# Optimization experiments

Hardware: AMD Instinct MI355X
Metric: run time of the kernel (lower is better)

Reference implementation:

```python
import jax, jax.numpy as jnp
import numpy as np

B, S, HID = 1, 2048, 1024
H, HKV, D = 16, 4, 64
THETA = 10000.0


def _rope_tables(seq_len, head_dim):
    # Matches RotaryEmbedding: emb = cat(freqs, freqs); kernel reads cos/sin at even
    # positions d for each rotated pair (d, d+1), i.e. columns 0::2 of the table.
    inv_freq = 1.0 / (THETA ** (jnp.arange(0, head_dim, 2, dtype=jnp.float32) / head_dim))
    freqs = jnp.arange(seq_len, dtype=jnp.float32)[:, None] * inv_freq[None, :]  # [S, D/2]
    emb = jnp.concatenate([freqs, freqs], axis=-1)  # [S, D]
    return jnp.cos(emb)[:, 0::2], jnp.sin(emb)[:, 0::2]  # each [S, D/2]


def _apply_rope(x, cos, sin):
    # x: [B, H, S, D]; rotate interleaved pairs (2i, 2i+1) as in the kernel.
    xe, xo = x[..., 0::2], x[..., 1::2]
    re = xe * cos - xo * sin
    ro = xe * sin + xo * cos
    return jnp.stack([re, ro], axis=-1).reshape(x.shape)


def setup_inputs() -> dict:
    key = jax.random.key(0)
    k0, k1, k2, k3, k4 = jax.random.split(key, 5)
    return {
        "hidden_states": jax.random.normal(k0, (B, S, HID), dtype=jnp.float32),
        "Wq": jax.random.normal(k1, (HID, H * D), dtype=jnp.float32) * 0.02,
        "Wk": jax.random.normal(k2, (HID, HKV * D), dtype=jnp.float32) * 0.02,
        "Wv": jax.random.normal(k3, (HID, HKV * D), dtype=jnp.float32) * 0.02,
        "Wo": jax.random.normal(k4, (H * D, HID), dtype=jnp.float32) * 0.02,
    }


def reference(hidden_states, Wq, Wk, Wv, Wo):
    b, s, _ = hidden_states.shape
    q = (hidden_states @ Wq).reshape(b, s, H, D).transpose(0, 2, 1, 3)    # [B,H,S,D]
    k = (hidden_states @ Wk).reshape(b, s, HKV, D).transpose(0, 2, 1, 3)  # [B,Hkv,S,D]
    v = (hidden_states @ Wv).reshape(b, s, HKV, D).transpose(0, 2, 1, 3)

    cos, sin = _rope_tables(s, D)
    q = _apply_rope(q, cos, sin)
    k = _apply_rope(k, cos, sin)

    G = H // HKV  # GQA group size: query head h -> kv head h // G
    qg = q.reshape(b, HKV, G, s, D)
    scale = jnp.float32(D) ** -0.5
    scores = jnp.einsum("bkgqd,bkpd->bkgqp", qg, k) * scale  # [B,Hkv,G,S,S]
    causal = jnp.tril(jnp.ones((s, s), dtype=bool))
    scores = jnp.where(causal, scores, jnp.float32(-1e30))
    probs = jax.nn.softmax(scores, axis=-1)
    out = jnp.einsum("bkgqp,bkpd->bkgqd", probs, v).reshape(b, H, s, D)
    out = out.transpose(0, 2, 1, 3).reshape(b, s, H * D)
    return out @ Wo
```

## Files before the change

kernel.cpp:

```cpp
#include <hip/hip_runtime.h>
#include <hip/hip_bf16.h>
#include <math.h>

#define SEQ   2048
#define HID   1024
#define NH    16
#define NKV   4
#define DH    64
#define GQ    (NH / NKV)
#define NQKV  1536
#define LQKV  1536
#define KT    64
#define QB    32
#define CH    512
#define NCH   (SEQ / CH)
#define PSTR  72

typedef __attribute__((ext_vector_type(8))) short bf16x8;
typedef __attribute__((ext_vector_type(4))) float f32x4;
typedef unsigned short u16;
typedef unsigned int u32;

__device__ __forceinline__ u16 f2bf(float f) {
    union { float f; unsigned u; } x; x.f = f;
    unsigned r = x.u + 0x7fffu + ((x.u >> 16) & 1u);
    return (u16)(r >> 16);
}
__device__ __forceinline__ u32 pk2bf(float lo, float hi) {
    return (u32)f2bf(lo) | ((u32)f2bf(hi) << 16);
}
__device__ __forceinline__ void load_lds16(const u16* g, u16* l) {
    __builtin_amdgcn_global_load_lds(
        (const __attribute__((address_space(1))) unsigned int*)g,
        (__attribute__((address_space(3))) unsigned int*)l, 16, 0, 0);
}

__global__ __launch_bounds__(256) void setup(const float* __restrict__ X,
                                             const float* __restrict__ Wq,
                                             const float* __restrict__ Wk,
                                             const float* __restrict__ Wv,
                                             const float* __restrict__ Wo,
                                             u16* __restrict__ Xb,
                                             u16* __restrict__ Wt,
                                             u16* __restrict__ WoT) {
    const int z = blockIdx.z;
    if (z == 4) {
        const int idx = ((int)blockIdx.y * 64 + (int)blockIdx.x) * 256 + threadIdx.x;
        const float4 v = ((const float4*)X)[idx];
        ushort4 o;
        o.x = f2bf(v.x); o.y = f2bf(v.y); o.z = f2bf(v.z); o.w = f2bf(v.w);
        ((ushort4*)Xb)[idx] = o;
        return;
    }
    const float* in; u16* out; int N;
    if (z == 0)      { in = Wq; out = Wt;                             N = HID; }
    else if (z == 1) { in = Wk; out = Wt + (size_t)HID * HID;         N = 256; }
    else if (z == 2) { in = Wv; out = Wt + (size_t)(HID + 256) * HID; N = 256; }
    else             { in = Wo; out = WoT;                            N = HID; }

    const int n0 = blockIdx.x * 32;
    if (n0 >= N) return;
    const int k0 = blockIdx.y * 32;

    __shared__ float t[32][33];
    const int tx = threadIdx.x & 31;
    const int ty = threadIdx.x >> 5;
    #pragma unroll
    for (int i = 0; i < 4; ++i)
        t[ty + i * 8][tx] = in[(size_t)(k0 + ty + i * 8) * N + n0 + tx];
    __syncthreads();
    #pragma unroll
    for (int i = 0; i < 4; ++i)
        out[(size_t)(n0 + ty + i * 8) * HID + k0 + tx] = f2bf(t[tx][ty + i * 8]);
}

__global__ __launch_bounds__(256) void gemm64(const u16* __restrict__ A,
                                              const u16* __restrict__ Bt,
                                              float* __restrict__ C,
                                              int K, int ldc) {
    __shared__ u16 Bs[2][64 * 32];

    const int tid  = threadIdx.x;
    const int lane = tid & 63;
    const int w    = tid >> 6;
    const int c    = lane & 15;
    const int quad = lane >> 4;
    const int m0   = blockIdx.y * 64;
    const int n0   = blockIdx.x * 64;

    const u16* gB  = Bt + (size_t)(n0 + w * 16 + (lane >> 2)) * K + (lane & 3) * 8;
    u16* const bdst = (u16*)&Bs[0][0] + (w * 16) * 32;

    const u16* gA = A + (size_t)(m0 + w * 16 + c) * K + quad * 8;

    const int T = K / 32;

    f32x4 acc[4];
    #pragma unroll
    for (int nt = 0; nt < 4; ++nt) acc[nt] = (f32x4){0.f, 0.f, 0.f, 0.f};

    bf16x8 afc, afn;
    afc = *(const bf16x8*)gA;
    load_lds16(gB, bdst);

    for (int t = 0; t < T; ++t) {
        __syncthreads();
        if (t + 1 < T) {
            load_lds16(gB + (t + 1) * 32, bdst + ((t + 1) & 1) * (64 * 32));
            afn = *(const bf16x8*)(gA + (t + 1) * 32);
        }
        bf16x8 bfr[4];
        #pragma unroll
        for (int nt = 0; nt < 4; ++nt)
            bfr[nt] = *(const bf16x8*)&Bs[t & 1][(nt * 16 + c) * 32 + quad * 8];
        #pragma unroll
        for (int nt = 0; nt < 4; ++nt)
            acc[nt] = __builtin_amdgcn_mfma_f32_16x16x32_bf16(afc, bfr[nt], acc[nt], 0, 0, 0);
        afc = afn;
    }

    #pragma unroll
    for (int nt = 0; nt < 4; ++nt)
        #pragma unroll
        for (int rg = 0; rg < 4; ++rg)
            C[(size_t)(m0 + w * 16 + quad * 4 + rg) * ldc + n0 + nt * 16 + c] = acc[nt][rg];
}

__global__ __launch_bounds__(256) void postprocess(const float* __restrict__ QKV,
                                                   u16* __restrict__ Qb,
                                                   u16* __restrict__ Kb,
                                                   u16* __restrict__ VTg) {
    const int s   = blockIdx.x;
    const int tid = threadIdx.x;
    const float* row = QKV + (size_t)s * LQKV;
    const float ln_scale = 9.210340371976184f / 32.0f;

    #pragma unroll
    for (int it = 0; it < 2; ++it) {
        const int p = tid + it * 256;
        const int j = p & 31;
        const float inv_freq = __expf(-(float)((2 * j) & 31) * ln_scale);
        float sn, cs;
        __sincosf((float)s * inv_freq, &sn, &cs);
        const float xe = row[2 * p], xo = row[2 * p + 1];
        Qb[(size_t)s * HID + 2 * p]     = f2bf((xe * cs - xo * sn) * 0.125f);
        Qb[(size_t)s * HID + 2 * p + 1] = f2bf((xe * sn + xo * cs) * 0.125f);
    }
    if (tid < 128) {
        const int p  = tid;
        const int j  = p & 31;
        const int kh = p >> 5;
        const int d  = (2 * p) & 63;
        const float inv_freq = __expf(-(float)((2 * j) & 31) * ln_scale);
        float sn, cs;
        __sincosf((float)s * inv_freq, &sn, &cs);
        const float xe = row[1024 + 2 * p], xo = row[1024 + 2 * p + 1];
        u16* kr = Kb + ((size_t)kh * SEQ + s) * DH;
        kr[d]     = f2bf(xe * cs - xo * sn);
        kr[d + 1] = f2bf(xe * sn + xo * cs);
    }
    {
        const int c = tid;
        const int kh = c >> 6, d = c & 63;
        VTg[((size_t)kh * DH + d) * SEQ + s] = f2bf(row[1280 + c]);
    }
}

__global__ __launch_bounds__(256) void attn_kernel(const u16* __restrict__ Qb,
                                                   const u16* __restrict__ Kb,
                                                   const u16* __restrict__ VTg,
                                                   float* __restrict__ Opart,
                                                   float* __restrict__ lpart) {
    __shared__ u16 Kst[64 * PSTR];
    __shared__ u16 VTst[64 * PSTR];
    __shared__ u16 Pst[4][QB * PSTR];

    const int tid  = threadIdx.x;
    const int lane = tid & 63;
    const int w    = tid >> 6;
    const int c    = lane & 15;
    const int quad = lane >> 4;
    const int kh   = blockIdx.y;
    const int z    = blockIdx.z;
    const int qt   = (SEQ / QB - 1) - (int)blockIdx.x;
    const int q0   = qt * QB;
    const int h    = kh * GQ + w;

    const int kstart = z * CH;
    const int klim   = q0 + QB;
    if (kstart >= klim) return;
    const int kend   = (klim < kstart + CH) ? klim : (kstart + CH);
    const int ntiles = (kend - kstart + KT - 1) / KT;

    bf16x8 qf[2][2];
    #pragma unroll
    for (int g = 0; g < 2; ++g)
        #pragma unroll
        for (int ks = 0; ks < 2; ++ks)
            qf[g][ks] = *(const bf16x8*)&Qb[(size_t)(q0 + g * 16 + c) * HID + h * DH + ks * 32 + quad * 8];

    f32x4 accO[4][2];
    #pragma unroll
    for (int nt = 0; nt < 4; ++nt)
        #pragma unroll
        for (int g = 0; g < 2; ++g)
            accO[nt][g] = (f32x4){0.f, 0.f, 0.f, 0.f};
    float l[2] = {0.f, 0.f};

    for (int t = 0; t < ntiles; ++t) {
        const int kt0 = kstart + t * KT;
        __syncthreads();
        {
            const int r = tid >> 3, off = (tid & 7) * 8;
            const u16* kg = &Kb[((size_t)kh * SEQ + kt0 + r) * DH + off];
            *(uint4*)&Kst[r * PSTR + off]        = *(const uint4*)kg;
            *(uint4*)&Kst[(r + 32) * PSTR + off] = *(const uint4*)(kg + 32 * DH);
            const u16* vg = &VTg[((size_t)kh * DH + r) * SEQ + kt0 + off];
            *(uint4*)&VTst[r * PSTR + off]        = *(const uint4*)vg;
            *(uint4*)&VTst[(r + 32) * PSTR + off] = *(const uint4*)(vg + 32 * SEQ);
        }
        __syncthreads();

        f32x4 accS[4][2];
        #pragma unroll
        for (int nS = 0; nS < 4; ++nS)
            #pragma unroll
            for (int g = 0; g < 2; ++g)
                accS[nS][g] = (f32x4){0.f, 0.f, 0.f, 0.f};
        #pragma unroll
        for (int nS = 0; nS < 4; ++nS)
            #pragma unroll
            for (int ks = 0; ks < 2; ++ks) {
                const bf16x8 kf = *(const bf16x8*)&Kst[(nS * 16 + c) * PSTR + ks * 32 + quad * 8];
                #pragma unroll
                for (int g = 0; g < 2; ++g)
                    accS[nS][g] = __builtin_amdgcn_mfma_f32_16x16x32_bf16(kf, qf[g][ks], accS[nS][g], 0, 0, 0);
            }

        #pragma unroll
        for (int g = 0; g < 2; ++g) {
            const int q = q0 + g * 16 + c;
            #pragma unroll
            for (int nS = 0; nS < 4; ++nS) {
                const int key = kt0 + nS * 16 + quad * 4;
                const float p0 = (key + 0 <= q) ? __expf(accS[nS][g][0]) : 0.f;
                const float p1 = (key + 1 <= q) ? __expf(accS[nS][g][1]) : 0.f;
                const float p2 = (key + 2 <= q) ? __expf(accS[nS][g][2]) : 0.f;
                const float p3 = (key + 3 <= q) ? __expf(accS[nS][g][3]) : 0.f;
                l[g] += (p0 + p1) + (p2 + p3);
                u32* dst = (u32*)&Pst[w][(g * 16 + c) * PSTR + nS * 16 + quad * 4];
                dst[0] = pk2bf(p0, p1);
                dst[1] = pk2bf(p2, p3);
            }
        }
        __threadfence_block();

        #pragma unroll
        for (int ks2 = 0; ks2 < 2; ++ks2) {
            bf16x8 pf[2];
            #pragma unroll
            for (int g = 0; g < 2; ++g)
                pf[g] = *(const bf16x8*)&Pst[w][(g * 16 + c) * PSTR + ks2 * 32 + quad * 8];
            #pragma unroll
            for (int nt = 0; nt < 4; ++nt) {
                const bf16x8 vf = *(const bf16x8*)&VTst[(nt * 16 + c) * PSTR + ks2 * 32 + quad * 8];
                #pragma unroll
                for (int g = 0; g < 2; ++g)
                    accO[nt][g] = __builtin_amdgcn_mfma_f32_16x16x32_bf16(vf, pf[g], accO[nt][g], 0, 0, 0);
            }
        }
    }

    #pragma unroll
    for (int g = 0; g < 2; ++g) {
        float lg = l[g];
        lg += __shfl_xor(lg, 16);
        lg += __shfl_xor(lg, 32);
        if (quad == 0)
            lpart[((size_t)z * SEQ + q0 + g * 16 + c) * NH + h] = lg;

        float* Op = Opart + ((size_t)z * SEQ + q0 + g * 16 + c) * HID + h * DH;
        #pragma unroll
        for (int nt = 0; nt < 4; ++nt)
            *(f32x4*)&Op[nt * 16 + quad * 4] = accO[nt][g];
    }
}

__global__ __launch_bounds__(256) void attn_reduce(const float* __restrict__ Opart,
                                                   const float* __restrict__ lpart,
                                                   u16* __restrict__ At) {
    const int idx = blockIdx.x * 256 + threadIdx.x;
    const int q  = idx >> 8;
    const int h  = (idx & 255) >> 4;
    const int klim = (q & ~(QB - 1)) + QB;
    float4 o = ((const float4*)Opart)[idx];
    float  l = lpart[q * NH + h];
    #pragma unroll
    for (int z = 1; z < NCH; ++z) {
        if (z * CH < klim) {
            const float4 o1 = ((const float4*)Opart)[idx + z * (SEQ * HID / 4)];
            o.x += o1.x; o.y += o1.y; o.z += o1.z; o.w += o1.w;
            l += lpart[(z * SEQ + q) * NH + h];
        }
    }
    const float inv = 1.0f / l;
    ushort4 r;
    r.x = f2bf(o.x * inv); r.y = f2bf(o.y * inv);
    r.z = f2bf(o.z * inv); r.w = f2bf(o.w * inv);
    ((ushort4*)At)[idx] = r;
}

extern "C" void kernel_launch(void* const* d_in, const int* in_sizes, int n_in,
                              void* d_out, int out_size, void* d_ws, size_t ws_size,
                              hipStream_t stream) {
    const float* X  = (const float*)d_in[0];
    const float* Wq = (const float*)d_in[1];
    const float* Wk = (const float*)d_in[2];
    const float* Wv = (const float*)d_in[3];
    const float* Wo = (const float*)d_in[4];
    float* out = (float*)d_out;

    u16* Wt     = (u16*)d_ws;
    u16* WoT    = Wt + (size_t)NQKV * HID;
    u16* Xb     = WoT + (size_t)HID * HID;
    u16* At     = Xb + (size_t)SEQ * HID;
    u16* Qb     = At + (size_t)SEQ * HID;
    u16* Kb     = Qb + (size_t)SEQ * HID;
    u16* VTg    = Kb + (size_t)NKV * SEQ * DH;
    float* QKVc = (float*)(VTg + (size_t)NKV * DH * SEQ);
    float* Opart = QKVc;
    float* lpart = Opart + (size_t)NCH * SEQ * HID;

    dim3 blk(256);

    setup<<<dim3(64, 32, 5), blk, 0, stream>>>(X, Wq, Wk, Wv, Wo, Xb, Wt, WoT);

    gemm64<<<dim3(NQKV / 64, SEQ / 64), blk, 0, stream>>>(Xb, Wt, QKVc, HID, LQKV);

    postprocess<<<SEQ, blk, 0, stream>>>(QKVc, Qb, Kb, VTg);

    attn_kernel<<<dim3(SEQ / QB, NKV, NCH), blk, 0, stream>>>(Qb, Kb, VTg, Opart, lpart);

    attn_reduce<<<(SEQ * HID / 4) / 256, blk, 0, stream>>>(Opart, lpart, At);

    gemm64<<<dim3(HID / 64, SEQ / 64), blk, 0, stream>>>(At, WoT, out, HID, HID);
}
```

Baseline: 154.1 us.

## Fuse RoPE and QKV layout into GEMM epilogue; double-buffer attention K/V loads

The QKV projection GEMM now applies RoPE, the Q scaling and the bf16 conversion in its epilogue, using a lane shuffle to fetch each rotation partner. It writes Q, K and transposed V straight to their final layouts, which drops the fp32 QKV intermediate and the separate postprocess kernel. The attention kernel also moves K/V tile staging to async global-to-LDS loads, double-buffered so the next tile is prefetched during compute, and removes one barrier per tile. The risks are uncoalesced scattered bf16 stores in the GEMM epilogue and LDS bank conflicts from the now unpadded K/V tiles.

```diff
diff --git a/kernel.cpp b/kernel.cpp
--- a/kernel.cpp
+++ b/kernel.cpp
@@ -9,12 +9,12 @@
 #define DH    64
 #define GQ    (NH / NKV)
 #define NQKV  1536
-#define LQKV  1536
 #define KT    64
 #define QB    32
 #define CH    512
 #define NCH   (SEQ / CH)
 #define PSTR  72
+#define LNSC  0.2878231366f
 
 typedef __attribute__((ext_vector_type(8))) short bf16x8;
 typedef __attribute__((ext_vector_type(4))) float f32x4;
@@ -74,10 +74,11 @@
         out[(size_t)(n0 + ty + i * 8) * HID + k0 + tx] = f2bf(t[tx][ty + i * 8]);
 }
 
-__global__ __launch_bounds__(256) void gemm64(const u16* __restrict__ A,
-                                              const u16* __restrict__ Bt,
-                                              float* __restrict__ C,
-                                              int K, int ldc) {
+__global__ __launch_bounds__(256) void gemm_qkv(const u16* __restrict__ A,
+                                                const u16* __restrict__ Bt,
+                                                u16* __restrict__ Qb,
+                                                u16* __restrict__ Kb,
+                                                u16* __restrict__ VTg) {
     __shared__ u16 Bs[2][64 * 32];
 
     const int tid  = threadIdx.x;
@@ -88,9 +89,86 @@
     const int m0   = blockIdx.y * 64;
     const int n0   = blockIdx.x * 64;
 
+    const u16* gB  = Bt + (size_t)(n0 + w * 16 + (lane >> 2)) * HID + (lane & 3) * 8;
+    u16* const bdst = (u16*)&Bs[0][0] + (w * 16) * 32;
+    const u16* gA = A + (size_t)(m0 + w * 16 + c) * HID + quad * 8;
+
+    f32x4 acc[4];
+    #pragma unroll
+    for (int nt = 0; nt < 4; ++nt) acc[nt] = (f32x4){0.f, 0.f, 0.f, 0.f};
+
+    bf16x8 afc, afn;
+    afc = *(const bf16x8*)gA;
+    load_lds16(gB, bdst);
+
+    for (int t = 0; t < HID / 32; ++t) {
+        __syncthreads();
+        if (t + 1 < HID / 32) {
+            load_lds16(gB + (t + 1) * 32, bdst + ((t + 1) & 1) * (64 * 32));
+            afn = *(const bf16x8*)(gA + (t + 1) * 32);
+        }
+        bf16x8 bfr[4];
+        #pragma unroll
+        for (int nt = 0; nt < 4; ++nt)
+            bfr[nt] = *(const bf16x8*)&Bs[t & 1][(nt * 16 + c) * 32 + quad * 8];
+        #pragma unroll
+        for (int nt = 0; nt < 4; ++nt)
+            acc[nt] = __builtin_amdgcn_mfma_f32_16x16x32_bf16(afc, bfr[nt], acc[nt], 0, 0, 0);
+        afc = afn;
+    }
+
+    const int s0 = m0 + w * 16 + quad * 4;
+    if (n0 < 1280) {
+        const bool isQ = (n0 < 1024);
+        #pragma unroll
+        for (int nt = 0; nt < 4; ++nt) {
+            const int d = nt * 16 + c;
+            const float inv_freq = __expf(-(float)(d & 30) * LNSC);
+            const float sgn = (d & 1) ? 1.f : -1.f;
+            #pragma unroll
+            for (int rg = 0; rg < 4; ++rg) {
+                const float self = acc[nt][rg];
+                const float partner = __shfl_xor(self, 1);
+                float sn, cs;
+                __sincosf((float)(s0 + rg) * inv_freq, &sn, &cs);
+                float o = fmaf(partner, sgn * sn, self * cs);
+                if (isQ) {
+                    Qb[(size_t)(s0 + rg) * HID + n0 + d] = f2bf(o * 0.125f);
+                } else {
+                    const int kh = (n0 - 1024) >> 6;
+                    Kb[((size_t)kh * SEQ + s0 + rg) * DH + d] = f2bf(o);
+                }
+            }
+        }
+    } else {
+        const int kh = (n0 - 1280) >> 6;
+        #pragma unroll
+        for (int nt = 0; nt < 4; ++nt) {
+            const int d = nt * 16 + c;
+            ushort4 o;
+            o.x = f2bf(acc[nt][0]); o.y = f2bf(acc[nt][1]);
+            o.z = f2bf(acc[nt][2]); o.w = f2bf(acc[nt][3]);
+            *(ushort4*)&VTg[((size_t)kh * DH + d) * SEQ + s0] = o;
+        }
+    }
+}
+
+__global__ __launch_bounds__(256) void gemm64(const u16* __restrict__ A,
+                                              const u16* __restrict__ Bt,
+                                              float* __restrict__ C,
+                                              int K, int ldc) {
+    __shared__ u16 Bs[2][64 * 32];
+
+    const int tid  = threadIdx.x;
+    const int lane = tid & 63;
+    const int w    = tid >> 6;
+    const int c    = lane & 15;
+    const int quad = lane >> 4;
+    const int m0   = blockIdx.y * 64;
+    const int n0   = blockIdx.x * 64;
+
     const u16* gB  = Bt + (size_t)(n0 + w * 16 + (lane >> 2)) * K + (lane & 3) * 8;
     u16* const bdst = (u16*)&Bs[0][0] + (w * 16) * 32;
-
     const u16* gA = A + (size_t)(m0 + w * 16 + c) * K + quad * 8;
 
     const int T = K / 32;
@@ -126,53 +204,13 @@
             C[(size_t)(m0 + w * 16 + quad * 4 + rg) * ldc + n0 + nt * 16 + c] = acc[nt][rg];
 }
 
-__global__ __launch_bounds__(256) void postprocess(const float* __restrict__ QKV,
-                                                   u16* __restrict__ Qb,
-                                                   u16* __restrict__ Kb,
-                                                   u16* __restrict__ VTg) {
-    const int s   = blockIdx.x;
-    const int tid = threadIdx.x;
-    const float* row = QKV + (size_t)s * LQKV;
-    const float ln_scale = 9.210340371976184f / 32.0f;
-
-    #pragma unroll
-    for (int it = 0; it < 2; ++it) {
-        const int p = tid + it * 256;
-        const int j = p & 31;
-        const float inv_freq = __expf(-(float)((2 * j) & 31) * ln_scale);
-        float sn, cs;
-        __sincosf((float)s * inv_freq, &sn, &cs);
-        const float xe = row[2 * p], xo = row[2 * p + 1];
-        Qb[(size_t)s * HID + 2 * p]     = f2bf((xe * cs - xo * sn) * 0.125f);
-        Qb[(size_t)s * HID + 2 * p + 1] = f2bf((xe * sn + xo * cs) * 0.125f);
-    }
-    if (tid < 128) {
-        const int p  = tid;
-        const int j  = p & 31;
-        const int kh = p >> 5;
-        const int d  = (2 * p) & 63;
-        const float inv_freq = __expf(-(float)((2 * j) & 31) * ln_scale);
-        float sn, cs;
-        __sincosf((float)s * inv_freq, &sn, &cs);
-        const float xe = row[1024 + 2 * p], xo = row[1024 + 2 * p + 1];
-        u16* kr = Kb + ((size_t)kh * SEQ + s) * DH;
-        kr[d]     = f2bf(xe * cs - xo * sn);
-        kr[d + 1] = f2bf(xe * sn + xo * cs);
-    }
-    {
-        const int c = tid;
-        const int kh = c >> 6, d = c & 63;
-        VTg[((size_t)kh * DH + d) * SEQ + s] = f2bf(row[1280 + c]);
-    }
-}
-
 __global__ __launch_bounds__(256) void attn_kernel(const u16* __restrict__ Qb,
                                                    const u16* __restrict__ Kb,
                                                    const u16* __restrict__ VTg,
                                                    float* __restrict__ Opart,
                                                    float* __restrict__ lpart) {
-    __shared__ u16 Kst[64 * PSTR];
-    __shared__ u16 VTst[64 * PSTR];
+    __shared__ u16 Ks[2][2][64 * 32];
+    __shared__ u16 Vs[2][2][64 * 32];
     __shared__ u16 Pst[4][QB * PSTR];
 
     const int tid  = threadIdx.x;
@@ -207,19 +245,38 @@
             accO[nt][g] = (f32x4){0.f, 0.f, 0.f, 0.f};
     float l[2] = {0.f, 0.f};
 
+    const int hf = w >> 1;
+    const int g0 = (w & 1) * 2;
+    const int srow = (lane >> 2);
+    const int scol = (lane & 3) * 8;
+
+    {
+        #pragma unroll
+        for (int gi = 0; gi < 2; ++gi) {
+            const int g = g0 + gi;
+            load_lds16(Kb + ((size_t)kh * SEQ + kstart + g * 16 + srow) * DH + hf * 32 + scol,
+                       &Ks[0][hf][(g * 16) * 32]);
+            load_lds16(VTg + ((size_t)kh * DH + g * 16 + srow) * SEQ + kstart + hf * 32 + scol,
+                       &Vs[0][hf][(g * 16) * 32]);
+        }
+    }
+
     for (int t = 0; t < ntiles; ++t) {
         const int kt0 = kstart + t * KT;
         __syncthreads();
-        {
-            const int r = tid >> 3, off = (tid & 7) * 8;
-            const u16* kg = &Kb[((size_t)kh * SEQ + kt0 + r) * DH + off];
-            *(uint4*)&Kst[r * PSTR + off]        = *(const uint4*)kg;
-            *(uint4*)&Kst[(r + 32) * PSTR + off] = *(const uint4*)(kg + 32 * DH);
-            const u16* vg = &VTg[((size_t)kh * DH + r) * SEQ + kt0 + off];
-            *(uint4*)&VTst[r * PSTR + off]        = *(const uint4*)vg;
-            *(uint4*)&VTst[(r + 32) * PSTR + off] = *(const uint4*)(vg + 32 * SEQ);
-        }
-        __syncthreads();
+        if (t + 1 < ntiles) {
+            const int nk = kt0 + KT;
+            const int nb = (t + 1) & 1;
+            #pragma unroll
+            for (int gi = 0; gi < 2; ++gi) {
+                const int g = g0 + gi;
+                load_lds16(Kb + ((size_t)kh * SEQ + nk + g * 16 + srow) * DH + hf * 32 + scol,
+                           &Ks[nb][hf][(g * 16) * 32]);
+                load_lds16(VTg + ((size_t)kh * DH + g * 16 + srow) * SEQ + nk + hf * 32 + scol,
+                           &Vs[nb][hf][(g * 16) * 32]);
+            }
+        }
+        const int b = t & 1;
 
         f32x4 accS[4][2];
         #pragma unroll
@@ -231,7 +288,7 @@
         for (int nS = 0; nS < 4; ++nS)
             #pragma unroll
             for (int ks = 0; ks < 2; ++ks) {
-                const bf16x8 kf = *(const bf16x8*)&Kst[(nS * 16 + c) * PSTR + ks * 32 + quad * 8];
+                const bf16x8 kf = *(const bf16x8*)&Ks[b][ks][(nS * 16 + c) * 32 + quad * 8];
                 #pragma unroll
                 for (int g = 0; g < 2; ++g)
                     accS[nS][g] = __builtin_amdgcn_mfma_f32_16x16x32_bf16(kf, qf[g][ks], accS[nS][g], 0, 0, 0);
@@ -263,7 +320,7 @@
                 pf[g] = *(const bf16x8*)&Pst[w][(g * 16 + c) * PSTR + ks2 * 32 + quad * 8];
             #pragma unroll
             for (int nt = 0; nt < 4; ++nt) {
-                const bf16x8 vf = *(const bf16x8*)&VTst[(nt * 16 + c) * PSTR + ks2 * 32 + quad * 8];
+                const bf16x8 vf = *(const bf16x8*)&Vs[b][ks2][(nt * 16 + c) * 32 + quad * 8];
                 #pragma unroll
                 for (int g = 0; g < 2; ++g)
                     accO[nt][g] = __builtin_amdgcn_mfma_f32_16x16x32_bf16(vf, pf[g], accO[nt][g], 0, 0, 0);
@@ -327,17 +384,14 @@
     u16* Qb     = At + (size_t)SEQ * HID;
     u16* Kb     = Qb + (size_t)SEQ * HID;
     u16* VTg    = Kb + (size_t)NKV * SEQ * DH;
-    float* QKVc = (float*)(VTg + (size_t)NKV * DH * SEQ);
-    float* Opart = QKVc;
+    float* Opart = (float*)(VTg + (size_t)NKV * DH * SEQ);
     float* lpart = Opart + (size_t)NCH * SEQ * HID;
 
     dim3 blk(256);
 
     setup<<<dim3(64, 32, 5), blk, 0, stream>>>(X, Wq, Wk, Wv, Wo, Xb, Wt, WoT);
 
-    gemm64<<<dim3(NQKV / 64, SEQ / 64), blk, 0, stream>>>(Xb, Wt, QKVc, HID, LQKV);
-
-    postprocess<<<SEQ, blk, 0, stream>>>(QKVc, Qb, Kb, VTg);
+    gemm_qkv<<<dim3(NQKV / 64, SEQ / 64), blk, 0, stream>>>(Xb, Wt, Qb, Kb, VTg);
 
     attn_kernel<<<dim3(SEQ / QB, NKV, NCH), blk, 0, stream>>>(Qb, Kb, VTg, Opart, lpart);
 
```

Result: faster. 141.1 us (-8.4%).
